# Kernel tuning notes

Hardware: AMD Instinct MI355X
Metric: run time of the kernel (lower is better)

The kernel has to match this reference:

```python
import jax, jax.numpy as jnp
import numpy as np


def _ln(x, g, b, eps=1e-5):
    m = x.mean(-1, keepdims=True)
    v = x.var(-1, keepdims=True)
    return (x - m) / jnp.sqrt(v + eps) * g + b


def _causal_linear_attn(q, k, v, eps=1e-3):
    # q, k, v: (b, h, n, d). Matches lucidrains causal_linear_attn with bucket_size=1:
    # q -> softmax over feature dim, k -> exp, inclusive cumsum of k and k(outer)v over n.
    dh = q.shape[-1]
    q = jax.nn.softmax(q, axis=-1) * (dh ** -0.5)
    k = jnp.exp(k)
    k_cum = jnp.cumsum(k, axis=2)                                  # (b,h,n,d)
    ctx = jnp.cumsum(k[..., :, None] * v[..., None, :], axis=2)    # (b,h,n,d,d) running sum of k_i v_i^T
    d_inv = 1.0 / jnp.clip(jnp.einsum('bhnd,bhnd->bhn', k_cum, q), eps, None)
    return jnp.einsum('bhnd,bhnde->bhne', q, ctx) * d_inv[..., None]


def reference(x, ln1_g, ln1_b, Wq, Wk, Wv, Wo, bo, ln2_g, ln2_b, W1, b1, W2, b2, n_heads):
    depth = Wq.shape[0]
    B, N, D = x.shape
    H = int(n_heads)
    dh = D // H
    for i in range(depth):
        # --- pre-norm linear self-attention block ---
        xn = _ln(x, ln1_g[i], ln1_b[i])
        q = (xn @ Wq[i]).reshape(B, N, H, dh).transpose(0, 2, 1, 3)
        k = (xn @ Wk[i]).reshape(B, N, H, dh).transpose(0, 2, 1, 3)
        v = (xn @ Wv[i]).reshape(B, N, H, dh).transpose(0, 2, 1, 3)
        a = _causal_linear_attn(q, k, v)
        a = a.transpose(0, 2, 1, 3).reshape(B, N, D)
        x = x + a @ Wo[i] + bo[i]
        # --- pre-norm feed-forward block (mult=4, exact GELU) ---
        xn = _ln(x, ln2_g[i], ln2_b[i])
        x = x + jax.nn.gelu(xn @ W1[i] + b1[i], approximate=False) @ W2[i] + b2[i]
    return x


def setup_inputs() -> dict:
    key = jax.random.key(0)
    ks = jax.random.split(key, 8)
    B, N, D, H, depth = 2, 2048, 1024, 16, 2
    FF = 4 * D
    s = D ** -0.5
    x = jax.random.normal(ks[0], (B, N, D), dtype=jnp.float32)
    Wq = jax.random.normal(ks[1], (depth, D, D), dtype=jnp.float32) * s
    Wk = jax.random.normal(ks[2], (depth, D, D), dtype=jnp.float32) * s
    Wv = jax.random.normal(ks[3], (depth, D, D), dtype=jnp.float32) * s
    Wo = jax.random.normal(ks[4], (depth, D, D), dtype=jnp.float32) * s
    W1 = jax.random.normal(ks[5], (depth, D, FF), dtype=jnp.float32) * s
    W2 = jax.random.normal(ks[6], (depth, FF, D), dtype=jnp.float32) * (FF ** -0.5)
    return dict(
        x=x,
        ln1_g=jnp.ones((depth, D), jnp.float32), ln1_b=jnp.zeros((depth, D), jnp.float32),
        Wq=Wq, Wk=Wk, Wv=Wv, Wo=Wo, bo=jnp.zeros((depth, D), jnp.float32),
        ln2_g=jnp.ones((depth, D), jnp.float32), ln2_b=jnp.zeros((depth, D), jnp.float32),
        W1=W1, b1=jnp.zeros((depth, FF), jnp.float32),
        W2=W2, b2=jnp.zeros((depth, D), jnp.float32),
        n_heads=H,
    )
```

## Files before the change

### kernel.cpp

```cpp
#include <hip/hip_runtime.h>
#include <cmath>

#define BB 2
#define SEQ 2048
#define DIM 1024
#define NH 16
#define DH 64
#define DEPTH 2
#define FFD 4096
#define CHK 64
#define NCHK (SEQ/CHK)
#define ROWS (BB*SEQ)
#define QKP (3*DIM)

typedef __bf16 bf16x8 __attribute__((ext_vector_type(8)));
typedef __bf16 bf16x4 __attribute__((ext_vector_type(4)));
typedef float  f32x4  __attribute__((ext_vector_type(4)));

#define AS1 __attribute__((address_space(1)))
#define AS3 __attribute__((address_space(3)))
#define FENCE() asm volatile("" ::: "memory")
#define LGKM0() asm volatile("s_waitcnt lgkmcnt(0)" ::: "memory")

template<int N> __device__ __forceinline__ void vmcnt_wait() {
    if constexpr (N == 0) asm volatile("s_waitcnt vmcnt(0)" ::: "memory");
    else if constexpr (N == 3) asm volatile("s_waitcnt vmcnt(3)" ::: "memory");
    else if constexpr (N == 4) asm volatile("s_waitcnt vmcnt(4)" ::: "memory");
    else if constexpr (N == 5) asm volatile("s_waitcnt vmcnt(5)" ::: "memory");
    else asm volatile("s_waitcnt vmcnt(6)" ::: "memory");
}

__device__ __forceinline__ float gelu_fast(float x) {
    float x3 = x * x * x;
    float y = 1.5957691216057308f * (x + 0.044715f * x3);
    return x * __builtin_amdgcn_rcpf(1.0f + __expf(-y));
}

__device__ __forceinline__ int swz128(int row, int col) {
    return row * 64 + (col ^ ((row & 7) << 3));
}

__device__ __forceinline__ void swz_tile(int bid, int NX, int NY, int& tx, int& ty) {
    int NB = NX * NY;
    int q = NB >> 3, r = NB & 7;
    int xcd = bid & 7, seq = bid >> 3;
    int start = (xcd < r) ? xcd * (q + 1) : r * (q + 1) + (xcd - r) * q;
    int wgid = start + seq;
    int g = 0, rem = wgid;
    int gw = (NX < 4) ? NX : 4;
    while (rem >= gw * NY) {
        rem -= gw * NY; g++;
        int left = NX - 4 * g;
        gw = left < 4 ? left : 4;
    }
    ty = rem / gw;
    tx = 4 * g + rem % gw;
}

__global__ __launch_bounds__(256) void ln_kernel(
    const float* __restrict__ x, const float* __restrict__ g,
    const float* __restrict__ b, __bf16* __restrict__ out)
{
    int row = blockIdx.x;
    const float4* xr = (const float4*)(x + (size_t)row * DIM);
    int t = threadIdx.x;
    float4 v = xr[t];
    float s  = v.x + v.y + v.z + v.w;
    float ss = v.x*v.x + v.y*v.y + v.z*v.z + v.w*v.w;
    #pragma unroll
    for (int off = 32; off > 0; off >>= 1) {
        s  += __shfl_down(s, off);
        ss += __shfl_down(ss, off);
    }
    __shared__ float wsum[4], wsq[4], stats[2];
    int wid = t >> 6, lane = t & 63;
    if (lane == 0) { wsum[wid] = s; wsq[wid] = ss; }
    __syncthreads();
    if (t == 0) {
        float S  = wsum[0] + wsum[1] + wsum[2] + wsum[3];
        float SS = wsq[0] + wsq[1] + wsq[2] + wsq[3];
        float mean = S * (1.0f / DIM);
        float var  = SS * (1.0f / DIM) - mean * mean;
        stats[0] = mean;
        stats[1] = rsqrtf(var + 1e-5f);
    }
    __syncthreads();
    float mean = stats[0], rstd = stats[1];
    float4 gv = ((const float4*)g)[t];
    float4 bv = ((const float4*)b)[t];
    bf16x4 o;
    o[0] = (__bf16)((v.x - mean) * rstd * gv.x + bv.x);
    o[1] = (__bf16)((v.y - mean) * rstd * gv.y + bv.y);
    o[2] = (__bf16)((v.z - mean) * rstd * gv.z + bv.z);
    o[3] = (__bf16)((v.w - mean) * rstd * gv.w + bv.w);
    *(bf16x4*)(out + (size_t)row * DIM + t * 4) = o;
}

__global__ __launch_bounds__(256) void transpose_all(
    const float* __restrict__ wq, const float* __restrict__ wk,
    const float* __restrict__ wv, const float* __restrict__ wo,
    const float* __restrict__ w1, const float* __restrict__ w2,
    __bf16* __restrict__ wqkt, __bf16* __restrict__ wot,
    __bf16* __restrict__ w1t, __bf16* __restrict__ w2t)
{
    int id = blockIdx.x;
    const float* W; __bf16* Wt; int K, N, txt, tyt;
    if (id < 4096) {
        int seg = id >> 10, r = id & 1023;
        K = DIM; N = DIM;
        txt = r & 31; tyt = r >> 5;
        W  = seg == 0 ? wq : seg == 1 ? wk : seg == 2 ? wv : wo;
        Wt = seg < 3 ? wqkt + (size_t)seg * DIM * DIM : wot;
    } else if (id < 8192) {
        int r = id - 4096;
        K = DIM; N = FFD;
        txt = r & 127; tyt = r >> 7;
        W = w1; Wt = w1t;
    } else {
        int r = id - 8192;
        K = FFD; N = DIM;
        txt = r & 31; tyt = r >> 5;
        W = w2; Wt = w2t;
    }
    __shared__ float tile[32][33];
    int bx = txt * 32, by = tyt * 32;
    int tx = threadIdx.x & 31, ty = threadIdx.x >> 5;
    #pragma unroll
    for (int i = 0; i < 32; i += 8)
        tile[ty + i][tx] = W[(size_t)(by + ty + i) * N + bx + tx];
    __syncthreads();
    #pragma unroll
    for (int i = 0; i < 32; i += 8)
        Wt[(size_t)(bx + ty + i) * K + by + tx] = (__bf16)tile[tx][ty + i];
}

__global__ __launch_bounds__(256) void transpose_v(
    const __bf16* __restrict__ qkv, __bf16* __restrict__ vT)
{
    __shared__ __bf16 tile[64 * 64];
    int bx = blockIdx.x;
    int by = blockIdx.y;
    int t = threadIdx.x;
    int r0 = t >> 3, sl = t & 7;
    #pragma unroll
    for (int i = 0; i < 2; i++) {
        int row = i * 32 + r0;
        bf16x8 d = *(const bf16x8*)(qkv + (size_t)(bx * 64 + row) * QKP + 2 * DIM + by * 64 + sl * 8);
        *(bf16x8*)&tile[row * 64 + ((sl ^ (row & 7)) << 3)] = d;
    }
    __syncthreads();
    #pragma unroll
    for (int i = 0; i < 2; i++) {
        int d = i * 32 + r0;
        int rbase = sl * 8;
        bf16x8 o;
        #pragma unroll
        for (int j = 0; j < 8; j++) {
            int rr = rbase + j;
            o[j] = tile[rr * 64 + (((((d >> 3)) ^ (rr & 7)) << 3) | (d & 7))];
        }
        *(bf16x8*)(vT + (size_t)(by * 64 + d) * ROWS + bx * 64 + rbase) = o;
    }
}

#define TBM 256
#define TBK 64
template<int MODE, int OUTBF, int NBF>
__global__ __launch_bounds__(512) void gemm256(
    const __bf16* __restrict__ A, const __bf16* __restrict__ Bt,
    void* __restrict__ Cv, const float* __restrict__ bias,
    const float* __restrict__ res, int M, int N, int K, int Kp,
    int NXT, int NYT, int NS)
{
    constexpr int ASZ = TBM * TBK;
    constexpr int BSZ = NBF * 64 * TBK;
    constexpr int VM4 = (NBF == 4) ? 4 : 3;
    constexpr int VM8 = (NBF == 4) ? 6 : 5;
    __shared__ __bf16 lds[2 * (ASZ + BSZ)];
    int nb = NXT * NYT;
    int sk = blockIdx.x / nb;
    int tx, ty;
    swz_tile(blockIdx.x % nb, NXT, NYT, tx, ty);
    if (NS > 1) {
        A  += (size_t)sk * K;
        Bt += (size_t)sk * K;
        Cv = (void*)((char*)Cv + (size_t)sk * M * N * (OUTBF ? 2 : 4));
    }
    const int bm = ty * TBM, bn = tx * (NBF * 64);
    const int t = threadIdx.x;
    const int l = t & 63, w = t >> 6;
    const int wm = w >> 2, wn = w & 3;
    const int lm = l & 15, lk = l >> 4;

    f32x4 acc[8][NBF] = {};
    const int nt = K / TBK;
    const int NIT = nt / 2;

    auto Aoff = [&](int bf) { return bf * (ASZ + BSZ); };
    auto Boff = [&](int bf) { return bf * (ASZ + BSZ) + ASZ; };

    const int s7 = lm & 7;
    const int c0 = (lk ^ s7) << 3;
    const int c1 = ((4 ^ lk) ^ s7) << 3;
    const __bf16* pA[2][2] = {
        { &lds[Aoff(0) + (wm * 128 + lm) * 64 + c0], &lds[Aoff(0) + (wm * 128 + lm) * 64 + c1] },
        { &lds[Aoff(1) + (wm * 128 + lm) * 64 + c0], &lds[Aoff(1) + (wm * 128 + lm) * 64 + c1] } };
    const __bf16* pB[2][2] = {
        { &lds[Boff(0) + (wn * (NBF * 16) + lm) * 64 + c0], &lds[Boff(0) + (wn * (NBF * 16) + lm) * 64 + c1] },
        { &lds[Boff(1) + (wn * (NBF * 16) + lm) * 64 + c0], &lds[Boff(1) + (wn * (NBF * 16) + lm) * 64 + c1] } };

    const int srow0 = t >> 3;
    const int scol0 = ((t & 7) ^ (srow0 & 7)) * 8;
    const __bf16* gAb = A + (size_t)(bm + srow0) * Kp + scol0;
    const __bf16* gBb = Bt + (size_t)(bn + srow0) * Kp + scol0;
    const int ldsw = w * 512;

    auto STAGEA_H = [&](int bf, int hf, int kt) {
        #pragma unroll
        for (int i = 0; i < 2; i++) {
            int u = hf * 2 + i;
            __builtin_amdgcn_global_load_lds(
                (const AS1 void*)(gAb + (size_t)(u * 64) * Kp + kt * 64),
                (AS3 void*)(&lds[Aoff(bf) + u * 4096 + ldsw]), 16, 0, 0);
        }
    };
    auto STAGEB_H = [&](int bf, int hf, int kt) {
        const int cnt = (NBF == 4) ? 2 : (hf == 0 ? 2 : 1);
        const int u0  = (NBF == 4) ? hf * 2 : (hf == 0 ? 0 : 2);
        #pragma unroll
        for (int i = 0; i < 2; i++) {
            if (i < cnt) {
                int u = u0 + i;
                __builtin_amdgcn_global_load_lds(
                    (const AS1 void*)(gBb + (size_t)(u * 64) * Kp + kt * 64),
                    (AS3 void*)(&lds[Boff(bf) + u * 4096 + ldsw]), 16, 0, 0);
            }
        }
    };
    auto LDA = [&](int bf, int g, bf16x8* aH) {
        #pragma unroll
        for (int j = 0; j < 4; j++) {
            aH[j * 2 + 0] = *(const bf16x8*)(pA[bf][0] + (g * 4 + j) * 1024);
            aH[j * 2 + 1] = *(const bf16x8*)(pA[bf][1] + (g * 4 + j) * 1024);
        }
    };
    auto LDB0 = [&](int bf, bf16x8* b0) {
        #pragma unroll
        for (int n = 0; n < 2; n++) {
            b0[n * 2 + 0] = *(const bf16x8*)(pB[bf][0] + n * 1024);
            b0[n * 2 + 1] = *(const bf16x8*)(pB[bf][1] + n * 1024);
        }
    };
    auto LDB1 = [&](int bf, bf16x8* b1) {
        #pragma unroll
        for (int n = 0; n < NBF - 2; n++) {
            b1[n * 2 + 0] = *(const bf16x8*)(pB[bf][0] + (2 + n) * 1024);
            b1[n * 2 + 1] = *(const bf16x8*)(pB[bf][1] + (2 + n) * 1024);
        }
    };
    auto MMQ0 = [&](int g, bf16x8* aH, bf16x8* b0) {
        __builtin_amdgcn_s_setprio(1);
        #pragma unroll
        for (int j = 0; j < 4; j++)
            #pragma unroll
            for (int nn = 0; nn < 2; nn++)
                #pragma unroll
                for (int kk = 0; kk < 2; kk++)
                    acc[g * 4 + j][nn] = __builtin_amdgcn_mfma_f32_16x16x32_bf16(
                        aH[j * 2 + kk], b0[nn * 2 + kk], acc[g * 4 + j][nn], 0, 0, 0);
        __builtin_amdgcn_s_setprio(0);
    };
    auto MMQ1 = [&](int g, bf16x8* aH, bf16x8* b1) {
        __builtin_amdgcn_s_setprio(1);
        #pragma unroll
        for (int j = 0; j < 4; j++)
            #pragma unroll
            for (int nn = 0; nn < NBF - 2; nn++)
                #pragma unroll
                for (int kk = 0; kk < 2; kk++)
                    acc[g * 4 + j][2 + nn] = __builtin_amdgcn_mfma_f32_16x16x32_bf16(
                        aH[j * 2 + kk], b1[nn * 2 + kk], acc[g * 4 + j][2 + nn], 0, 0, 0);
        __builtin_amdgcn_s_setprio(0);
    };

    STAGEA_H(0, 0, 0); STAGEA_H(0, 1, 0); STAGEB_H(0, 0, 0); STAGEB_H(0, 1, 0);
    STAGEB_H(1, 0, 1); STAGEB_H(1, 1, 1); STAGEA_H(1, 0, 1);
    vmcnt_wait<VM8>();
    __builtin_amdgcn_s_barrier();

    bf16x8 aH[8], bH0[4], bH1[2 * (NBF - 2)];
    for (int it = 0; it < NIT; it++) {
        int u = 2 * it + 1, T2 = 2 * it + 2, U2 = 2 * it + 3;
        LDA(0, 0, aH); LDB0(0, bH0);
        STAGEA_H(1, 1, u);
        FENCE(); __builtin_amdgcn_s_barrier();
        LGKM0();
        MMQ0(0, aH, bH0);
        FENCE(); __builtin_amdgcn_s_barrier();
        LDB1(0, bH1);
        FENCE(); __builtin_amdgcn_s_barrier();
        LGKM0();
        MMQ1(0, aH, bH1);
        FENCE(); __builtin_amdgcn_s_barrier();
        LDA(0, 1, aH);
        if (T2 < nt) STAGEB_H(0, 0, T2);
        FENCE(); __builtin_amdgcn_s_barrier();
        LGKM0();
        MMQ1(1, aH, bH1);
        FENCE(); __builtin_amdgcn_s_barrier();
        if (T2 < nt) {
            STAGEB_H(0, 1, T2);
            vmcnt_wait<VM4>();
        } else {
            vmcnt_wait<0>();
        }
        __builtin_amdgcn_s_barrier();
        MMQ0(1, aH, bH0);
        FENCE(); __builtin_amdgcn_s_barrier();
        LDA(1, 0, aH); LDB0(1, bH0);
        if (T2 < nt) STAGEA_H(0, 0, T2);
        FENCE(); __builtin_amdgcn_s_barrier();
        LGKM0();
        MMQ0(0, aH, bH0);
        FENCE(); __builtin_amdgcn_s_barrier();
        LDB1(1, bH1);
        if (T2 < nt) STAGEA_H(0, 1, T2);
        FENCE(); __builtin_amdgcn_s_barrier();
        LGKM0();
        MMQ1(0, aH, bH1);
        FENCE(); __builtin_amdgcn_s_barrier();
        LDA(1, 1, aH);
        if (U2 < nt) { STAGEB_H(1, 0, U2); STAGEB_H(1, 1, U2); }
        FENCE(); __builtin_amdgcn_s_barrier();
        LGKM0();
        MMQ1(1, aH, bH1);
        FENCE(); __builtin_amdgcn_s_barrier();
        if (U2 < nt) {
            STAGEA_H(1, 0, U2);
            vmcnt_wait<VM8>();
        } else {
            vmcnt_wait<0>();
        }
        __builtin_amdgcn_s_barrier();
        MMQ0(1, aH, bH0);
        FENCE(); __builtin_amdgcn_s_barrier();
    }

    #pragma unroll
    for (int m = 0; m < 8; m++) {
        #pragma unroll
        for (int n = 0; n < NBF; n++) {
            int col = bn + wn * (NBF * 16) + n * 16 + lm;
            #pragma unroll
            for (int r = 0; r < 4; r++) {
                int row = bm + wm * 128 + m * 16 + lk * 4 + r;
                float v = acc[m][n][r];
                if (MODE == 1) v += res[(size_t)row * N + col] + bias[col];
                if (MODE == 2) v = gelu_fast(v + bias[col]);
                if (OUTBF) ((__bf16*)Cv)[(size_t)row * N + col] = (__bf16)v;
                else       ((float*)Cv)[(size_t)row * N + col] = v;
            }
        }
    }
}

template<int DOLN>
__global__ __launch_bounds__(256) void reduce4ln(
    const __bf16* __restrict__ parts, const float* __restrict__ bias,
    float* __restrict__ x, const float* __restrict__ g,
    const float* __restrict__ b, __bf16* __restrict__ xn)
{
    const size_t PS = (size_t)ROWS * DIM;
    int row = blockIdx.x, t = threadIdx.x;
    size_t base = (size_t)row * DIM + t * 4;
    float4 xr = *(const float4*)(x + base);
    float4 bv = ((const float4*)bias)[t];
    float o0 = xr.x + bv.x, o1 = xr.y + bv.y, o2 = xr.z + bv.z, o3 = xr.w + bv.w;
    #pragma unroll
    for (int s = 0; s < 4; s++) {
        bf16x4 p = *(const bf16x4*)(parts + s * PS + base);
        o0 += (float)p[0]; o1 += (float)p[1]; o2 += (float)p[2]; o3 += (float)p[3];
    }
    float4 o = {o0, o1, o2, o3};
    *(float4*)(x + base) = o;
    if constexpr (DOLN) {
        float s  = o0 + o1 + o2 + o3;
        float ss = o0*o0 + o1*o1 + o2*o2 + o3*o3;
        #pragma unroll
        for (int off = 32; off > 0; off >>= 1) {
            s  += __shfl_down(s, off);
            ss += __shfl_down(ss, off);
        }
        __shared__ float wsum[4], wsq[4], stats[2];
        int wid = t >> 6, lane = t & 63;
        if (lane == 0) { wsum[wid] = s; wsq[wid] = ss; }
        __syncthreads();
        if (t == 0) {
            float S  = wsum[0] + wsum[1] + wsum[2] + wsum[3];
            float SS = wsq[0] + wsq[1] + wsq[2] + wsq[3];
            float mean = S * (1.0f / DIM);
            float var  = SS * (1.0f / DIM) - mean * mean;
            stats[0] = mean;
            stats[1] = rsqrtf(var + 1e-5f);
        }
        __syncthreads();
        float mean = stats[0], rstd = stats[1];
        float4 gv = ((const float4*)g)[t];
        float4 bvv = ((const float4*)b)[t];
        bf16x4 on;
        on[0] = (__bf16)((o0 - mean) * rstd * gv.x + bvv.x);
        on[1] = (__bf16)((o1 - mean) * rstd * gv.y + bvv.y);
        on[2] = (__bf16)((o2 - mean) * rstd * gv.z + bvv.z);
        on[3] = (__bf16)((o3 - mean) * rstd * gv.w + bvv.w);
        *(bf16x4*)(xn + base) = on;
    }
}

__global__ __launch_bounds__(256) void attn_local_m(
    const __bf16* __restrict__ qkv, const __bf16* __restrict__ vTg,
    float* __restrict__ KVT, float* __restrict__ Ksum)
{
    int blk = blockIdx.x;
    int c = blk % NCHK, bh = blk / NCHK;
    int b = bh / NH, h = bh % NH;
    __shared__ __bf16 ek_s[64 * 64];
    __shared__ __bf16 ekT_s[64 * 68];
    __shared__ float ksum_p[4][64];
    int t = threadIdx.x, w = t >> 6, l = t & 63;
    size_t rowbase = (size_t)(b * SEQ + c * CHK);

    {
        int m = t >> 2, dq = t & 3;
        const __bf16* kr = qkv + (rowbase + m) * QKP + DIM + h * DH + dq * 16;
        bf16x8 k0 = *(const bf16x8*)kr;
        bf16x8 k1 = *(const bf16x8*)(kr + 8);
        bf16x8 e0, e1;
        #pragma unroll
        for (int j = 0; j < 8; j++) {
            e0[j] = (__bf16)__expf((float)k0[j]);
            e1[j] = (__bf16)__expf((float)k1[j]);
        }
        *(bf16x8*)&ek_s[swz128(m, dq * 16)] = e0;
        *(bf16x8*)&ek_s[swz128(m, dq * 16 + 8)] = e1;
    }
    __syncthreads();
    {
        float kacc = 0.f;
        #pragma unroll
        for (int g = 0; g < 4; g++) {
            bf16x4 pk;
            #pragma unroll
            for (int j = 0; j < 4; j++) {
                __bf16 e = ek_s[swz128(w * 16 + g * 4 + j, l)];
                pk[j] = e;
                kacc += (float)e;
            }
            *(bf16x4*)&ekT_s[l * 68 + w * 16 + g * 4] = pk;
        }
        ksum_p[w][l] = kacc;
    }
    __syncthreads();
    f32x4 acc[4] = {};
    const __bf16* vbase = vTg + (size_t)(h * DH + w * 16 + (l & 15)) * ROWS
                        + (size_t)b * SEQ + c * CHK + (l >> 4) * 8;
    bf16x8 a0 = *(const bf16x8*)vbase;
    bf16x8 a1 = *(const bf16x8*)(vbase + 32);
    #pragma unroll
    for (int fn = 0; fn < 4; fn++) {
        int rbase = (fn * 16 + (l & 15)) * 68 + (l >> 4) * 8;
        bf16x4 b0a = *(const bf16x4*)&ekT_s[rbase];
        bf16x4 b0b = *(const bf16x4*)&ekT_s[rbase + 4];
        bf16x4 b1a = *(const bf16x4*)&ekT_s[rbase + 32];
        bf16x4 b1b = *(const bf16x4*)&ekT_s[rbase + 36];
        bf16x8 b0, b1;
        #pragma unroll
        for (int j = 0; j < 4; j++) {
            b0[j] = b0a[j]; b0[j + 4] = b0b[j];
            b1[j] = b1a[j]; b1[j + 4] = b1b[j];
        }
        acc[fn] = __builtin_amdgcn_mfma_f32_16x16x32_bf16(a0, b0, acc[fn], 0, 0, 0);
        acc[fn] = __builtin_amdgcn_mfma_f32_16x16x32_bf16(a1, b1, acc[fn], 0, 0, 0);
    }
    float* kvout = KVT + (size_t)(bh * NCHK + c) * (DH * DH);
    #pragma unroll
    for (int fn = 0; fn < 4; fn++)
        #pragma unroll
        for (int r = 0; r < 4; r++)
            kvout[(w * 16 + (l >> 4) * 4 + r) * DH + fn * 16 + (l & 15)] = acc[fn][r];
    if (t < 64) {
        float s = ksum_p[0][t] + ksum_p[1][t] + ksum_p[2][t] + ksum_p[3][t];
        Ksum[(size_t)(bh * NCHK + c) * DH + t] = s;
    }
}

__global__ __launch_bounds__(256) void attn_scan2(
    float* __restrict__ KV, float* __restrict__ Ksum)
{
    int bh = blockIdx.y;
    int bx = blockIdx.x;
    int t = threadIdx.x;
    if (bx < 16) {
        int elem = bx * 256 + t;
        float run = 0.f;
        for (int c = 0; c < NCHK; c++) {
            float* p = KV + ((size_t)(bh * NCHK + c)) * (DH * DH) + elem;
            float tmp = *p;
            *p = run;
            run += tmp;
        }
    } else if (t < DH) {
        float run = 0.f;
        for (int c = 0; c < NCHK; c++) {
            float* p = Ksum + ((size_t)(bh * NCHK + c)) * DH + t;
            float tmp = *p;
            *p = run;
            run += tmp;
        }
    }
}

__global__ __launch_bounds__(256) void attn_out_m(
    const __bf16* __restrict__ qkv, const __bf16* __restrict__ vTg,
    const float* __restrict__ KVT, const float* __restrict__ Ksum,
    __bf16* __restrict__ ag)
{
    int blk = blockIdx.x;
    int c = blk % NCHK, bh = blk / NCHK;
    int b = bh / NH, h = bh % NH;
    __shared__ __bf16 q_s[64 * 64];
    __shared__ __bf16 ek_s[64 * 64];
    __shared__ __bf16 s_s[64 * 64];
    __shared__ __bf16 kvT_s[64 * 64];
    __shared__ float denom_s[64];
    int t = threadIdx.x, w = t >> 6, l = t & 63;
    size_t rowbase = (size_t)(b * SEQ + c * CHK);

    {
        int i = t >> 2, dq = t & 3;
        const __bf16* qr = qkv + (rowbase + i) * QKP + h * DH + dq * 16;
        bf16x8 q0 = *(const bf16x8*)qr, q1 = *(const bf16x8*)(qr + 8);
        float qf[16];
        #pragma unroll
        for (int j = 0; j < 8; j++) { qf[j] = (float)q0[j]; qf[8 + j] = (float)q1[j]; }
        float mx = qf[0];
        #pragma unroll
        for (int j = 1; j < 16; j++) mx = fmaxf(mx, qf[j]);
        mx = fmaxf(mx, __shfl_xor(mx, 1));
        mx = fmaxf(mx, __shfl_xor(mx, 2));
        float ss = 0.f;
        #pragma unroll
        for (int j = 0; j < 16; j++) { qf[j] = __expf(qf[j] - mx); ss += qf[j]; }
        ss += __shfl_xor(ss, 1);
        ss += __shfl_xor(ss, 2);
        float sc = 0.125f / ss;
        bf16x8 o0, o1;
        #pragma unroll
        for (int j = 0; j < 8; j++) {
            o0[j] = (__bf16)(qf[j] * sc);
            o1[j] = (__bf16)(qf[8 + j] * sc);
        }
        *(bf16x8*)&q_s[swz128(i, dq * 16)] = o0;
        *(bf16x8*)&q_s[swz128(i, dq * 16 + 8)] = o1;
        const float* kp = Ksum + (size_t)(bh * NCHK + c) * DH + dq * 16;
        float dk = 0.f;
        #pragma unroll
        for (int j = 0; j < 16; j++) dk += (qf[j] * sc) * kp[j];
        dk += __shfl_xor(dk, 1);
        dk += __shfl_xor(dk, 2);
        if (dq == 0) denom_s[i] = dk;
    }
    {
        int m = t >> 2, dq = t & 3;
        const __bf16* kr = qkv + (rowbase + m) * QKP + DIM + h * DH + dq * 16;
        bf16x8 k0 = *(const bf16x8*)kr, k1 = *(const bf16x8*)(kr + 8);
        bf16x8 e0, e1;
        #pragma unroll
        for (int j = 0; j < 8; j++) {
            e0[j] = (__bf16)__expf((float)k0[j]);
            e1[j] = (__bf16)__expf((float)k1[j]);
        }
        *(bf16x8*)&ek_s[swz128(m, dq * 16)] = e0;
        *(bf16x8*)&ek_s[swz128(m, dq * 16 + 8)] = e1;
    }
    {
        int e = t >> 2, dq = t & 3;
        const float* kvr = KVT + (size_t)(bh * NCHK + c) * (DH * DH) + e * DH + dq * 16;
        bf16x8 o0, o1;
        #pragma unroll
        for (int j = 0; j < 8; j++) { o0[j] = (__bf16)kvr[j]; o1[j] = (__bf16)kvr[8 + j]; }
        *(bf16x8*)&kvT_s[swz128(e, dq * 16)] = o0;
        *(bf16x8*)&kvT_s[swz128(e, dq * 16 + 8)] = o1;
    }
    __syncthreads();

    bf16x8 bq0 = *(const bf16x8*)&q_s[swz128(w * 16 + (l & 15), (l >> 4) * 8)];
    bf16x8 bq1 = *(const bf16x8*)&q_s[swz128(w * 16 + (l & 15), 32 + (l >> 4) * 8)];
    int i_col = w * 16 + (l & 15);
    float dsum = 0.f;
    #pragma unroll
    for (int fm = 0; fm < 4; fm++) {
        bf16x8 ae0 = *(const bf16x8*)&ek_s[swz128(fm * 16 + (l & 15), (l >> 4) * 8)];
        bf16x8 ae1 = *(const bf16x8*)&ek_s[swz128(fm * 16 + (l & 15), 32 + (l >> 4) * 8)];
        f32x4 z = {};
        z = __builtin_amdgcn_mfma_f32_16x16x32_bf16(ae0, bq0, z, 0, 0, 0);
        z = __builtin_amdgcn_mfma_f32_16x16x32_bf16(ae1, bq1, z, 0, 0, 0);
        bf16x4 pk;
        #pragma unroll
        for (int r = 0; r < 4; r++) {
            int m = fm * 16 + (l >> 4) * 4 + r;
            float v = (m <= i_col) ? z[r] : 0.f;
            pk[r] = (__bf16)v;
            dsum += (float)pk[r];
        }
        *(bf16x4*)&s_s[swz128(i_col, fm * 16 + (l >> 4) * 4)] = pk;
    }
    dsum += __shfl_xor(dsum, 16);
    dsum += __shfl_xor(dsum, 32);
    if (l < 16) denom_s[w * 16 + l] += dsum;

    bf16x8 as0 = *(const bf16x8*)&s_s[swz128(w * 16 + (l & 15), (l >> 4) * 8)];
    bf16x8 as1 = *(const bf16x8*)&s_s[swz128(w * 16 + (l & 15), 32 + (l >> 4) * 8)];
    f32x4 oacc[4] = {};
    #pragma unroll
    for (int fn = 0; fn < 4; fn++) {
        const __bf16* vb = vTg + (size_t)(h * DH + fn * 16 + (l & 15)) * ROWS
                         + (size_t)b * SEQ + c * CHK + (l >> 4) * 8;
        bf16x8 bv0 = *(const bf16x8*)vb;
        bf16x8 bv1 = *(const bf16x8*)(vb + 32);
        bf16x8 bk0 = *(const bf16x8*)&kvT_s[swz128(fn * 16 + (l & 15), (l >> 4) * 8)];
        bf16x8 bk1 = *(const bf16x8*)&kvT_s[swz128(fn * 16 + (l & 15), 32 + (l >> 4) * 8)];
        f32x4 z = oacc[fn];
        z = __builtin_amdgcn_mfma_f32_16x16x32_bf16(as0, bv0, z, 0, 0, 0);
        z = __builtin_amdgcn_mfma_f32_16x16x32_bf16(as1, bv1, z, 0, 0, 0);
        z = __builtin_amdgcn_mfma_f32_16x16x32_bf16(bq0, bk0, z, 0, 0, 0);
        z = __builtin_amdgcn_mfma_f32_16x16x32_bf16(bq1, bk1, z, 0, 0, 0);
        oacc[fn] = z;
    }
    #pragma unroll
    for (int r = 0; r < 4; r++) {
        int i = w * 16 + (l >> 4) * 4 + r;
        float dinv = 1.0f / fmaxf(denom_s[i], 1e-3f);
        #pragma unroll
        for (int fn = 0; fn < 4; fn++)
            ag[(rowbase + i) * DIM + h * DH + fn * 16 + (l & 15)] = (__bf16)(oacc[fn][r] * dinv);
    }
}

extern "C" void kernel_launch(void* const* d_in, const int* in_sizes, int n_in,
                              void* d_out, int out_size, void* d_ws, size_t ws_size,
                              hipStream_t stream) {
    (void)in_sizes; (void)n_in; (void)out_size; (void)ws_size;
    const float* x_in  = (const float*)d_in[0];
    const float* ln1_g = (const float*)d_in[1];
    const float* ln1_b = (const float*)d_in[2];
    const float* Wq    = (const float*)d_in[3];
    const float* Wk    = (const float*)d_in[4];
    const float* Wv    = (const float*)d_in[5];
    const float* Wo    = (const float*)d_in[6];
    const float* bo    = (const float*)d_in[7];
    const float* ln2_g = (const float*)d_in[8];
    const float* ln2_b = (const float*)d_in[9];
    const float* W1    = (const float*)d_in[10];
    const float* b1    = (const float*)d_in[11];
    const float* W2    = (const float*)d_in[12];
    const float* b2    = (const float*)d_in[13];

    float* x = (float*)d_out;
    const size_t MB = 1024 * 1024;
    char* base = (char*)d_ws;

    __bf16* qkv    = (__bf16*)base;
    __bf16* partsO = (__bf16*)base;
    __bf16* h1     = (__bf16*)base;
    __bf16* vTg    = (__bf16*)(base + 24 * MB);
    __bf16* xn     = (__bf16*)(base + 32 * MB);
    __bf16* parts  = (__bf16*)(base + 32 * MB);
    __bf16* a      = (__bf16*)(base + 40 * MB);
    float*  KVT    = (float*)(base + 48 * MB);
    float*  Ks     = (float*)(base + 64 * MB);
    __bf16* wqkt   = (__bf16*)(base + 65 * MB);
    __bf16* wot    = (__bf16*)(base + 71 * MB);
    __bf16* w1t    = (__bf16*)(base + 73 * MB);
    __bf16* w2t    = (__bf16*)(base + 81 * MB);

    const size_t SZ = (size_t)ROWS * DIM;
    hipMemcpyAsync(x, x_in, SZ * sizeof(float), hipMemcpyDeviceToDevice, stream);

    dim3 gScan(17, BB * NH);
    dim3 gTv(ROWS / 64, DIM / 64);

    for (int l = 0; l < DEPTH; l++) {
        const float* wq = Wq + (size_t)l * DIM * DIM;
        const float* wk = Wk + (size_t)l * DIM * DIM;
        const float* wv = Wv + (size_t)l * DIM * DIM;
        const float* wo = Wo + (size_t)l * DIM * DIM;
        const float* w1 = W1 + (size_t)l * DIM * FFD;
        const float* w2 = W2 + (size_t)l * FFD * DIM;

        transpose_all<<<12288, 256, 0, stream>>>(wq, wk, wv, wo, w1, w2,
                                                 wqkt, wot, w1t, w2t);

        if (l == 0)
            ln_kernel<<<ROWS, 256, 0, stream>>>(x, ln1_g, ln1_b, xn);
        gemm256<0, 1, 3><<<16 * 16, 512, 0, stream>>>(xn, wqkt, qkv, nullptr, nullptr,
                                                      ROWS, QKP, DIM, DIM, 16, 16, 1);
        transpose_v<<<gTv, 256, 0, stream>>>(qkv, vTg);
        attn_local_m<<<BB * NH * NCHK, 256, 0, stream>>>(qkv, vTg, KVT, Ks);
        attn_scan2<<<gScan, 256, 0, stream>>>(KVT, Ks);
        attn_out_m<<<BB * NH * NCHK, 256, 0, stream>>>(qkv, vTg, KVT, Ks, a);
        gemm256<0, 1, 4><<<4 * 16 * 4, 512, 0, stream>>>(a, wot, partsO, nullptr, nullptr,
                                                         ROWS, DIM, DIM / 4, DIM, 4, 16, 4);
        reduce4ln<1><<<ROWS, 256, 0, stream>>>(partsO, bo + l * DIM, x,
                                               ln2_g + l * DIM, ln2_b + l * DIM, xn);

        gemm256<2, 1, 4><<<16 * 16, 512, 0, stream>>>(xn, w1t, h1, b1 + l * FFD, nullptr,
                                                      ROWS, FFD, DIM, DIM, 16, 16, 1);
        gemm256<0, 1, 4><<<4 * 16 * 4, 512, 0, stream>>>(h1, w2t, parts, nullptr, nullptr,
                                                         ROWS, DIM, FFD / 4, FFD, 4, 16, 4);
        if (l + 1 < DEPTH)
            reduce4ln<1><<<ROWS, 256, 0, stream>>>(parts, b2 + l * DIM, x,
                                                   ln1_g + (l + 1) * DIM,
                                                   ln1_b + (l + 1) * DIM, xn);
        else
            reduce4ln<0><<<ROWS, 256, 0, stream>>>(parts, b2 + l * DIM, x,
                                                   nullptr, nullptr, nullptr);
    }
}
```

Baseline: 390.5 us.

## Add 128x128 single-buffered GEMM for output projection and FF1, reduce split-K

```diff
diff --git a/kernel.cpp b/kernel.cpp
--- a/kernel.cpp
+++ b/kernel.cpp
@@ -163,6 +163,90 @@
     }
 }
 
+#define GBM 128
+#define GBN 128
+#define GBK 64
+template<int MODE, int OUTBF>
+__global__ __launch_bounds__(256) void gemm_m97(
+    const __bf16* __restrict__ A, const __bf16* __restrict__ Bt,
+    void* __restrict__ Cv, const float* __restrict__ bias,
+    const float* __restrict__ res, int M, int N, int K, int Kp,
+    int NXT, int NYT, int NS)
+{
+    __shared__ __bf16 Als[GBM * GBK];
+    __shared__ __bf16 Bls[GBN * GBK];
+    int nb = NXT * NYT;
+    int sk = blockIdx.x / nb;
+    int tx, ty;
+    swz_tile(blockIdx.x % nb, NXT, NYT, tx, ty);
+    if (NS > 1) {
+        A  += (size_t)sk * K;
+        Bt += (size_t)sk * K;
+        Cv = (void*)((char*)Cv + (size_t)sk * M * N * (OUTBF ? 2 : 4));
+    }
+    const int t = threadIdx.x;
+    const int lane = t & 63;
+    const int w = t >> 6;
+    const int wr = w >> 1, wc = w & 1;
+    const int bm = ty * GBM, bn = tx * GBN;
+
+    f32x4 acc[4][4] = {};
+
+    const int srow = w * 32 + (lane >> 3);
+    const int scol = (lane & 7) * 8;
+    const __bf16* gA = A + (size_t)(bm + srow) * Kp + scol;
+    const __bf16* gB = Bt + (size_t)(bn + srow) * Kp + scol;
+    __bf16* lA = Als + w * 2048;
+    __bf16* lB = Bls + w * 2048;
+
+    for (int k0 = 0; k0 < K; k0 += GBK) {
+        #pragma unroll
+        for (int i = 0; i < 4; i++) {
+            __builtin_amdgcn_global_load_lds(
+                (const AS1 void*)(gA + (size_t)(i * 8) * Kp + k0),
+                (AS3 void*)(lA + i * 512), 16, 0, 0);
+            __builtin_amdgcn_global_load_lds(
+                (const AS1 void*)(gB + (size_t)(i * 8) * Kp + k0),
+                (AS3 void*)(lB + i * 512), 16, 0, 0);
+        }
+        __syncthreads();
+        #pragma unroll
+        for (int kk = 0; kk < GBK; kk += 32) {
+            bf16x8 af[4], bfr[4];
+            #pragma unroll
+            for (int m = 0; m < 4; m++)
+                af[m] = *(const bf16x8*)&Als[(wr * 64 + m * 16 + (lane & 15)) * GBK + kk + (lane >> 4) * 8];
+            #pragma unroll
+            for (int n = 0; n < 4; n++)
+                bfr[n] = *(const bf16x8*)&Bls[(wc * 64 + n * 16 + (lane & 15)) * GBK + kk + (lane >> 4) * 8];
+            #pragma unroll
+            for (int m = 0; m < 4; m++)
+                #pragma unroll
+                for (int n = 0; n < 4; n++)
+                    acc[m][n] = __builtin_amdgcn_mfma_f32_16x16x32_bf16(af[m], bfr[n], acc[m][n], 0, 0, 0);
+        }
+        __syncthreads();
+    }
+    const int crow0 = bm + wr * 64 + (lane >> 4) * 4;
+    const int ccol0 = bn + wc * 64 + (lane & 15);
+    #pragma unroll
+    for (int m = 0; m < 4; m++) {
+        #pragma unroll
+        for (int n = 0; n < 4; n++) {
+            int col = ccol0 + n * 16;
+            #pragma unroll
+            for (int r = 0; r < 4; r++) {
+                int row = crow0 + m * 16 + r;
+                float v = acc[m][n][r];
+                if (MODE == 1) v += res[(size_t)row * N + col] + bias[col];
+                if (MODE == 2) v = gelu_fast(v + bias[col]);
+                if (OUTBF) ((__bf16*)Cv)[(size_t)row * N + col] = (__bf16)v;
+                else       ((float*)Cv)[(size_t)row * N + col] = v;
+            }
+        }
+    }
+}
+
 #define TBM 256
 #define TBK 64
 template<int MODE, int OUTBF, int NBF>
@@ -364,8 +448,8 @@
     }
 }
 
-template<int DOLN>
-__global__ __launch_bounds__(256) void reduce4ln(
+template<int NP, int DOLN>
+__global__ __launch_bounds__(256) void reduceNln(
     const __bf16* __restrict__ parts, const float* __restrict__ bias,
     float* __restrict__ x, const float* __restrict__ g,
     const float* __restrict__ b, __bf16* __restrict__ xn)
@@ -377,7 +461,7 @@
     float4 bv = ((const float4*)bias)[t];
     float o0 = xr.x + bv.x, o1 = xr.y + bv.y, o2 = xr.z + bv.z, o3 = xr.w + bv.w;
     #pragma unroll
-    for (int s = 0; s < 4; s++) {
+    for (int s = 0; s < NP; s++) {
         bf16x4 p = *(const bf16x4*)(parts + s * PS + base);
         o0 += (float)p[0]; o1 += (float)p[1]; o2 += (float)p[2]; o3 += (float)p[3];
     }
@@ -708,21 +792,21 @@
         attn_local_m<<<BB * NH * NCHK, 256, 0, stream>>>(qkv, vTg, KVT, Ks);
         attn_scan2<<<gScan, 256, 0, stream>>>(KVT, Ks);
         attn_out_m<<<BB * NH * NCHK, 256, 0, stream>>>(qkv, vTg, KVT, Ks, a);
-        gemm256<0, 1, 4><<<4 * 16 * 4, 512, 0, stream>>>(a, wot, partsO, nullptr, nullptr,
-                                                         ROWS, DIM, DIM / 4, DIM, 4, 16, 4);
-        reduce4ln<1><<<ROWS, 256, 0, stream>>>(partsO, bo + l * DIM, x,
-                                               ln2_g + l * DIM, ln2_b + l * DIM, xn);
-
-        gemm256<2, 1, 4><<<16 * 16, 512, 0, stream>>>(xn, w1t, h1, b1 + l * FFD, nullptr,
-                                                      ROWS, FFD, DIM, DIM, 16, 16, 1);
+        gemm_m97<0, 1><<<2 * 8 * 32, 256, 0, stream>>>(a, wot, partsO, nullptr, nullptr,
+                                                       ROWS, DIM, DIM / 2, DIM, 8, 32, 2);
+        reduceNln<2, 1><<<ROWS, 256, 0, stream>>>(partsO, bo + l * DIM, x,
+                                                  ln2_g + l * DIM, ln2_b + l * DIM, xn);
+
+        gemm_m97<2, 1><<<32 * 32, 256, 0, stream>>>(xn, w1t, h1, b1 + l * FFD, nullptr,
+                                                    ROWS, FFD, DIM, DIM, 32, 32, 1);
         gemm256<0, 1, 4><<<4 * 16 * 4, 512, 0, stream>>>(h1, w2t, parts, nullptr, nullptr,
                                                          ROWS, DIM, FFD / 4, FFD, 4, 16, 4);
         if (l + 1 < DEPTH)
-            reduce4ln<1><<<ROWS, 256, 0, stream>>>(parts, b2 + l * DIM, x,
-                                                   ln1_g + (l + 1) * DIM,
-                                                   ln1_b + (l + 1) * DIM, xn);
+            reduceNln<4, 1><<<ROWS, 256, 0, stream>>>(parts, b2 + l * DIM, x,
+                                                      ln1_g + (l + 1) * DIM,
+                                                      ln1_b + (l + 1) * DIM, xn);
         else
-            reduce4ln<0><<<ROWS, 256, 0, stream>>>(parts, b2 + l * DIM, x,
-                                                   nullptr, nullptr, nullptr);
-    }
-}
+            reduceNln<4, 0><<<ROWS, 256, 0, stream>>>(parts, b2 + l * DIM, x,
+                                                      nullptr, nullptr, nullptr);
+    }
+}
```

Measured after the change: 420.8 us. +7.7%, slower.
